# Performance work log

Measured on AMD Instinct MI355X. Metric: run time of the kernel, lower is better.

Reference implementation:

```python
import math
import jax, jax.numpy as jnp
import numpy as np

B, T, C = 2, 2048, 1024
H, Ca = 16, 64


def setup_inputs() -> dict:
    key = jax.random.key(0)
    ks = jax.random.split(key, 5)
    # kaiming-uniform-ish scale for weights
    wb = 1.0 / math.sqrt(C)
    return {
        "x": jax.random.normal(ks[0], (B, T, C), dtype=jnp.float32),
        "w_q": jax.random.uniform(ks[1], (H, C, Ca), jnp.float32, -wb, wb),
        "w_k": jax.random.uniform(ks[2], (H, C, Ca), jnp.float32, -wb, wb),
        "w_v": jax.random.uniform(ks[3], (H, C, Ca), jnp.float32, -wb, wb),
        "w_o": jax.random.uniform(ks[4], (C, C), jnp.float32, -wb, wb),
    }


def reference(x, w_q, w_k, w_v, w_o):
    # x: [B,T,C]; w_q/w_k/w_v: [H,C,Ca]; w_o: [C,C]
    scale = 1.0 / math.sqrt(w_q.shape[-1])
    q = jnp.einsum("btc,hca->bhta", x, w_q)  # [B,H,T,Ca]
    k = jnp.einsum("btc,hca->bhta", x, w_k)
    v = jnp.einsum("btc,hca->bhta", x, w_v)
    s = jnp.einsum("bhta,bhsa->bhts", q, k)  # [B,H,T,T]
    # faithful to original: mask where tril(s)==0, scale applied after masking
    s_hat = jnp.where(jnp.tril(s) == 0, -jnp.inf, s * scale)
    a = jax.nn.softmax(s_hat, axis=-1)
    y = jnp.einsum("bhts,bhsa->bhta", a, v)  # [B,H,T,Ca]
    y_cat = y.transpose(0, 2, 1, 3).reshape(x.shape)  # [B,T,C]
    return y_cat @ w_o
```

## Files before the change

### kernel.cpp

```cpp
#include <hip/hip_runtime.h>
#include <stdint.h>

#define Bc 2
#define Tc 2048
#define Cn 1024
#define Hc 16
#define CAc 64

typedef __attribute__((ext_vector_type(8))) short short8;
typedef __attribute__((ext_vector_type(4))) float f32x4;

__device__ __forceinline__ unsigned short f2bf(float f) {
    unsigned int u = __builtin_bit_cast(unsigned int, f);
    return (unsigned short)((u + 0x7fffu + ((u >> 16) & 1u)) >> 16);
}

__device__ __forceinline__ void async_cp16(const unsigned short* g, unsigned short* l) {
    __builtin_amdgcn_global_load_lds(
        (const __attribute__((address_space(1))) unsigned int*)g,
        (__attribute__((address_space(3))) unsigned int*)l,
        16, 0, 0);
}

__global__ __launch_bounds__(256) void detect_dtype(
    const unsigned short* __restrict__ x, int* __restrict__ flag)
{
    __shared__ int cnt;
    if (threadIdx.x == 0) cnt = 0;
    __syncthreads();
    int c = 0;
#pragma unroll
    for (int i = 0; i < 8; i++) {
        int idx = (threadIdx.x * 8 + i) * 2;
        unsigned short u = x[idx];
        int e = (u >> 7) & 0xFF;
        if (e >= 0x68 && e <= 0x90) c++;
    }
    atomicAdd(&cnt, c);
    __syncthreads();
    if (threadIdx.x == 0) *flag = (cnt > 1024) ? 1 : 0;
}

__global__ __launch_bounds__(256) void convert_x(
    const void* __restrict__ xin, unsigned short* __restrict__ xb,
    const int* __restrict__ flag)
{
    int idx = (blockIdx.x * 256 + threadIdx.x) * 4;
    if (*flag) {
        *(uint2*)(&xb[idx]) = *(const uint2*)((const unsigned short*)xin + idx);
    } else {
        const float* xf = (const float*)xin;
        float4 v = *(const float4*)(xf + idx);
        union { unsigned short s[4]; uint2 u; } p;
        p.s[0] = f2bf(v.x); p.s[1] = f2bf(v.y); p.s[2] = f2bf(v.z); p.s[3] = f2bf(v.w);
        *(uint2*)(&xb[idx]) = p.u;
    }
}

__device__ __forceinline__ unsigned short ld_elem(const void* base, size_t off, int isbf) {
    return isbf ? ((const unsigned short*)base)[off] : f2bf(((const float*)base)[off]);
}

__global__ __launch_bounds__(256) void transpose_weights(
    const void* __restrict__ wq, const void* __restrict__ wk,
    const void* __restrict__ wv, const void* __restrict__ wo,
    unsigned short* __restrict__ wT, unsigned short* __restrict__ woT,
    const int* __restrict__ flag)
{
    const int isbf = *flag;
    __shared__ unsigned short tile[32][33];
    const int bx = blockIdx.x;
    const int t = threadIdx.x;
    const int tx = t & 31, ty = t >> 5;
    const void* src;
    unsigned short* dst;
    int R, Cw, r0, c0;
    if (bx < 3072) {
        int g = bx >> 6;
        int rem = bx & 63;
        int ct = rem >> 1;
        int at = rem & 1;
        int proj = g >> 4, h = g & 15;
        const void* wsel = (proj == 0) ? wq : ((proj == 1) ? wk : wv);
        src = isbf ? (const void*)((const unsigned short*)wsel + (size_t)h * Cn * CAc)
                   : (const void*)((const float*)wsel + (size_t)h * Cn * CAc);
        dst = wT + (size_t)g * CAc * Cn;
        R = Cn; Cw = CAc; r0 = ct * 32; c0 = at * 32;
    } else {
        int rem = bx - 3072;
        src = wo; dst = woT;
        R = Cn; Cw = Cn;
        r0 = (rem >> 5) * 32; c0 = (rem & 31) * 32;
    }
#pragma unroll
    for (int j = 0; j < 4; j++)
        tile[ty + j * 8][tx] = ld_elem(src, (size_t)(r0 + ty + j * 8) * Cw + c0 + tx, isbf);
    __syncthreads();
#pragma unroll
    for (int j = 0; j < 4; j++)
        dst[(size_t)(c0 + ty + j * 8) * R + r0 + tx] = tile[tx][ty + j * 8];
}

template <int MODE>
__global__ __launch_bounds__(256) void gemm128(
    const unsigned short* __restrict__ Amat,
    const unsigned short* __restrict__ Bt,
    void* __restrict__ o0,
    unsigned short* __restrict__ o1,
    unsigned short* __restrict__ o2,
    const int* __restrict__ flag)
{
    __shared__ alignas(16) unsigned short Al[2][128 * 32];
    __shared__ alignas(16) unsigned short Bl[2][128 * 32];
    const int tid = threadIdx.x;
    const int wave = tid >> 6, lane = tid & 63;
    const int l15 = lane & 15, quad = lane >> 4;
    const int mBase = blockIdx.y * 128, nBase = blockIdx.x * 128;
    const int mOff = (wave & 1) * 64, nOff = (wave >> 1) * 64;

    const int srow = lane >> 2;
    const int sgc  = (lane & 3) ^ (srow & 3);
    const int sw = (quad ^ (l15 & 3)) * 8;

    f32x4 acc[4][4];
#pragma unroll
    for (int i = 0; i < 4; i++)
#pragma unroll
        for (int j = 0; j < 4; j++)
            acc[i][j] = (f32x4){0.f, 0.f, 0.f, 0.f};

#pragma unroll
    for (int t = 0; t < 2; t++) {
        int rl = wave * 32 + t * 16;
        async_cp16(Amat + (size_t)(mBase + rl + srow) * Cn + sgc * 8, &Al[0][rl * 32]);
        async_cp16(Bt   + (size_t)(nBase + rl + srow) * Cn + sgc * 8, &Bl[0][rl * 32]);
    }
    __syncthreads();

    for (int kk = 0; kk < 32; kk++) {
        const int cur = kk & 1;
        if (kk < 31) {
            const int k1 = (kk + 1) * 32;
#pragma unroll
            for (int t = 0; t < 2; t++) {
                int rl = wave * 32 + t * 16;
                async_cp16(Amat + (size_t)(mBase + rl + srow) * Cn + k1 + sgc * 8, &Al[1 - cur][rl * 32]);
                async_cp16(Bt   + (size_t)(nBase + rl + srow) * Cn + k1 + sgc * 8, &Bl[1 - cur][rl * 32]);
            }
        }
        short8 af[4], bfr[4];
#pragma unroll
        for (int i = 0; i < 4; i++)
            af[i] = *(const short8*)(&Al[cur][(mOff + i * 16 + l15) * 32 + sw]);
#pragma unroll
        for (int j = 0; j < 4; j++)
            bfr[j] = *(const short8*)(&Bl[cur][(nOff + j * 16 + l15) * 32 + sw]);
#pragma unroll
        for (int i = 0; i < 4; i++)
#pragma unroll
            for (int j = 0; j < 4; j++)
                acc[i][j] = __builtin_amdgcn_mfma_f32_16x16x32_bf16(af[i], bfr[j], acc[i][j], 0, 0, 0);
        __syncthreads();
    }

    if constexpr (MODE == 0) {
#pragma unroll
        for (int i = 0; i < 4; i++) {
            int m0 = mBase + mOff + i * 16 + quad * 4;
            int b = m0 >> 11, t0 = m0 & (Tc - 1);
#pragma unroll
            for (int j = 0; j < 4; j++) {
                int n = nBase + nOff + j * 16 + l15;
                int proj = n >> 10, h = (n >> 6) & 15, a = n & 63;
                if (proj == 2) {
                    union { unsigned short s[4]; uint2 v; } pk;
#pragma unroll
                    for (int r = 0; r < 4; r++) pk.s[r] = f2bf(acc[i][j][r]);
                    *(uint2*)(&o2[((size_t)(b * Hc + h) * CAc + a) * Tc + t0]) = pk.v;
                } else {
                    unsigned short* dst = (proj == 0) ? (unsigned short*)o0 : o1;
                    size_t base = ((size_t)(b * Hc + h) * Tc + t0) * CAc + a;
#pragma unroll
                    for (int r = 0; r < 4; r++)
                        dst[base + (size_t)r * CAc] = f2bf(acc[i][j][r]);
                }
            }
        }
    } else {
        const int isbf = *flag;
#pragma unroll
        for (int i = 0; i < 4; i++) {
            int m0 = mBase + mOff + i * 16 + quad * 4;
#pragma unroll
            for (int j = 0; j < 4; j++) {
                int n = nBase + nOff + j * 16 + l15;
                if (isbf) {
#pragma unroll
                    for (int r = 0; r < 4; r++)
                        ((unsigned short*)o0)[(size_t)(m0 + r) * Cn + n] = f2bf(acc[i][j][r]);
                } else {
#pragma unroll
                    for (int r = 0; r < 4; r++)
                        ((float*)o0)[(size_t)(m0 + r) * Cn + n] = acc[i][j][r];
                }
            }
        }
    }
}

__global__ __launch_bounds__(256) void attn_pair(
    const unsigned short* __restrict__ q,
    const unsigned short* __restrict__ k,
    const unsigned short* __restrict__ vT,
    unsigned short* __restrict__ y)
{
    __shared__ alignas(16) unsigned short Kl[2][64 * 64];
    __shared__ alignas(16) unsigned short Vl[2][64 * 64];
    const int LDP = 72;
    __shared__ alignas(16) unsigned short Pl[4][16 * LDP];
    const int bx = blockIdx.x;
    const int pr = bx & 15, bh = bx >> 4;
    const int h = bh & 15, b = bh >> 4;
    const int qt1 = pr, qt2 = 31 - pr;
    const int tid = threadIdx.x;
    const int wave = tid >> 6, lane = tid & 63;
    const int l15 = lane & 15, quad = lane >> 4;
    const int m0w1 = qt1 * 64 + wave * 16;
    const int m0w2 = qt2 * 64 + wave * 16;
    const size_t bhoff = (size_t)(b * Hc + h);
    const unsigned short* qh = q + bhoff * Tc * CAc;
    const unsigned short* kh = k + bhoff * Tc * CAc;
    const unsigned short* vh = vT + bhoff * CAc * Tc;

    const int srow = (lane >> 3);
    const int sgc  = (lane & 7) ^ srow;
    const int h7 = l15 & 7;
    const int sw0 = ((quad ^ h7) << 3);
    const int sw1 = (((4 + quad) ^ h7) << 3);

    short8 qf1[2], qf2[2];
#pragma unroll
    for (int s = 0; s < 2; s++) {
        qf1[s] = *(const short8*)(&qh[(size_t)(m0w1 + l15) * CAc + s * 32 + quad * 8]);
        qf2[s] = *(const short8*)(&qh[(size_t)(m0w2 + l15) * CAc + s * 32 + quad * 8]);
    }

    f32x4 oacc1[4], oacc2[4], osum1, osum2;
#pragma unroll
    for (int j2 = 0; j2 < 4; j2++) {
        oacc1[j2] = (f32x4){0.f, 0.f, 0.f, 0.f};
        oacc2[j2] = (f32x4){0.f, 0.f, 0.f, 0.f};
    }
    osum1 = (f32x4){0.f, 0.f, 0.f, 0.f};
    osum2 = (f32x4){0.f, 0.f, 0.f, 0.f};

    const unsigned short ONE = 0x3F80;
    short8 ones;
#pragma unroll
    for (int i = 0; i < 8; i++) ones[i] = (short)ONE;

    unsigned short* Pw = &Pl[wave][0];

#pragma unroll
    for (int t = 0; t < 2; t++) {
        int rl = wave * 16 + t * 8;
        async_cp16(kh + (size_t)(rl + srow) * CAc + sgc * 8, &Kl[0][rl * 64]);
        async_cp16(vh + (size_t)(rl + srow) * Tc  + sgc * 8, &Vl[0][rl * 64]);
    }
    __syncthreads();

    for (int kt = 0; kt <= qt2; kt++) {
        const int k0 = kt * 64;
        const int cur = kt & 1;
        const bool act1 = (kt <= qt1);
        if (kt < qt2) {
            const unsigned short* kg = kh + (size_t)(k0 + 64) * CAc;
            const unsigned short* vg = vh + (k0 + 64);
#pragma unroll
            for (int t = 0; t < 2; t++) {
                int rl = wave * 16 + t * 8;
                async_cp16(kg + (size_t)(rl + srow) * CAc + sgc * 8, &Kl[1 - cur][rl * 64]);
                async_cp16(vg + (size_t)(rl + srow) * Tc  + sgc * 8, &Vl[1 - cur][rl * 64]);
            }
        }
        const unsigned short* Kc = Kl[cur];
        const unsigned short* Vc = Vl[cur];

        float s1[4][4], s2[4][4];
#pragma unroll
        for (int j = 0; j < 4; j++) {
            short8 kf0 = *(const short8*)(&Kc[(j * 16 + l15) * 64 + sw0]);
            short8 kf1 = *(const short8*)(&Kc[(j * 16 + l15) * 64 + sw1]);
            f32x4 z2 = (f32x4){0.f, 0.f, 0.f, 0.f};
            z2 = __builtin_amdgcn_mfma_f32_16x16x32_bf16(kf0, qf2[0], z2, 0, 0, 0);
            z2 = __builtin_amdgcn_mfma_f32_16x16x32_bf16(kf1, qf2[1], z2, 0, 0, 0);
#pragma unroll
            for (int r = 0; r < 4; r++) s2[j][r] = z2[r];
            if (act1) {
                f32x4 z1 = (f32x4){0.f, 0.f, 0.f, 0.f};
                z1 = __builtin_amdgcn_mfma_f32_16x16x32_bf16(kf0, qf1[0], z1, 0, 0, 0);
                z1 = __builtin_amdgcn_mfma_f32_16x16x32_bf16(kf1, qf1[1], z1, 0, 0, 0);
#pragma unroll
                for (int r = 0; r < 4; r++) s1[j][r] = z1[r];
            }
        }

        if (kt == qt2) {
            int tg = m0w2 + l15;
#pragma unroll
            for (int j = 0; j < 4; j++)
#pragma unroll
                for (int r = 0; r < 4; r++) {
                    int sg = k0 + j * 16 + quad * 4 + r;
                    s2[j][r] = (sg <= tg) ? __expf(s2[j][r] * 0.125f) : 0.f;
                }
        } else {
#pragma unroll
            for (int j = 0; j < 4; j++)
#pragma unroll
                for (int r = 0; r < 4; r++)
                    s2[j][r] = __expf(s2[j][r] * 0.125f);
        }
        if (act1) {
            if (kt == qt1) {
                int tg = m0w1 + l15;
#pragma unroll
                for (int j = 0; j < 4; j++)
#pragma unroll
                    for (int r = 0; r < 4; r++) {
                        int sg = k0 + j * 16 + quad * 4 + r;
                        s1[j][r] = (sg <= tg) ? __expf(s1[j][r] * 0.125f) : 0.f;
                    }
            } else {
#pragma unroll
                for (int j = 0; j < 4; j++)
#pragma unroll
                    for (int r = 0; r < 4; r++)
                        s1[j][r] = __expf(s1[j][r] * 0.125f);
            }
        }

        short8 pa2[2], pa1[2];
#pragma unroll
        for (int j = 0; j < 4; j++) {
            union { unsigned int d[2]; uint2 v; } pk;
            pk.d[0] = (unsigned int)f2bf(s2[j][0]) | ((unsigned int)f2bf(s2[j][1]) << 16);
            pk.d[1] = (unsigned int)f2bf(s2[j][2]) | ((unsigned int)f2bf(s2[j][3]) << 16);
            *(uint2*)(&Pw[l15 * LDP + j * 16 + quad * 4]) = pk.v;
        }
#pragma unroll
        for (int c = 0; c < 2; c++)
            pa2[c] = *(const short8*)(&Pw[l15 * LDP + c * 32 + quad * 8]);
        if (act1) {
#pragma unroll
            for (int j = 0; j < 4; j++) {
                union { unsigned int d[2]; uint2 v; } pk;
                pk.d[0] = (unsigned int)f2bf(s1[j][0]) | ((unsigned int)f2bf(s1[j][1]) << 16);
                pk.d[1] = (unsigned int)f2bf(s1[j][2]) | ((unsigned int)f2bf(s1[j][3]) << 16);
                *(uint2*)(&Pw[l15 * LDP + j * 16 + quad * 4]) = pk.v;
            }
#pragma unroll
            for (int c = 0; c < 2; c++)
                pa1[c] = *(const short8*)(&Pw[l15 * LDP + c * 32 + quad * 8]);
        }

#pragma unroll
        for (int c = 0; c < 2; c++) {
#pragma unroll
            for (int j2 = 0; j2 < 4; j2++) {
                short8 vb = *(const short8*)(&Vc[(j2 * 16 + l15) * 64 + (c ? sw1 : sw0)]);
                oacc2[j2] = __builtin_amdgcn_mfma_f32_16x16x32_bf16(pa2[c], vb, oacc2[j2], 0, 0, 0);
                if (act1)
                    oacc1[j2] = __builtin_amdgcn_mfma_f32_16x16x32_bf16(pa1[c], vb, oacc1[j2], 0, 0, 0);
            }
            osum2 = __builtin_amdgcn_mfma_f32_16x16x32_bf16(pa2[c], ones, osum2, 0, 0, 0);
            if (act1)
                osum1 = __builtin_amdgcn_mfma_f32_16x16x32_bf16(pa1[c], ones, osum1, 0, 0, 0);
        }
        __syncthreads();
    }

    float ri1[4], ri2[4];
#pragma unroll
    for (int r = 0; r < 4; r++) { ri1[r] = 1.0f / osum1[r]; ri2[r] = 1.0f / osum2[r]; }
#pragma unroll
    for (int j2 = 0; j2 < 4; j2++) {
#pragma unroll
        for (int r = 0; r < 4; r++) {
            int t1 = m0w1 + quad * 4 + r;
            int t2 = m0w2 + quad * 4 + r;
            y[((size_t)b * Tc + t1) * Cn + h * CAc + j2 * 16 + l15] = f2bf(oacc1[j2][r] * ri1[r]);
            y[((size_t)b * Tc + t2) * Cn + h * CAc + j2 * 16 + l15] = f2bf(oacc2[j2][r] * ri2[r]);
        }
    }
}

extern "C" void kernel_launch(void* const* d_in, const int* in_sizes, int n_in,
                              void* d_out, int out_size, void* d_ws, size_t ws_size,
                              hipStream_t stream) {
    const void* x  = d_in[0];
    const void* wq = d_in[1];
    const void* wk = d_in[2];
    const void* wv = d_in[3];
    const void* wo = d_in[4];
    char* ws = (char*)d_ws;
    int* flag = (int*)(ws);
    unsigned short* wT  = (unsigned short*)(ws + ((size_t)1 << 20));
    unsigned short* woT = (unsigned short*)(ws + ((size_t)7 << 20));
    unsigned short* xb  = (unsigned short*)(ws + ((size_t)9 << 20));
    unsigned short* qb  = (unsigned short*)(ws + ((size_t)17 << 20));
    unsigned short* kb  = (unsigned short*)(ws + ((size_t)25 << 20));
    unsigned short* vTb = (unsigned short*)(ws + ((size_t)33 << 20));
    unsigned short* yb  = (unsigned short*)(ws + ((size_t)41 << 20));

    detect_dtype<<<dim3(1), dim3(256), 0, stream>>>((const unsigned short*)x, flag);
    convert_x<<<dim3(4096), dim3(256), 0, stream>>>(x, xb, flag);
    transpose_weights<<<dim3(4096), dim3(256), 0, stream>>>(wq, wk, wv, wo, wT, woT, flag);
    gemm128<0><<<dim3(24, 32), dim3(256), 0, stream>>>(xb, wT, qb, kb, vTb, flag);
    attn_pair<<<dim3(512), dim3(256), 0, stream>>>(qb, kb, vTb, yb);
    gemm128<1><<<dim3(8, 32), dim3(256), 0, stream>>>(yb, woT, d_out, nullptr, nullptr, flag);
}
```

Before: 211.8 us.

## Merge prep kernels, shrink output GEMM tile, truncate softmax probabilities to bf16

Fuses the x conversion and weight transpose into one launch to save a kernel launch and its gap. The output projection now uses 64x128 tiles, giving 512 blocks instead of 256 so more of the GPU's compute units are filled. In attention, probabilities are packed to bf16 by truncation instead of round-to-nearest, which cuts ALU work in the inner loop but adds a small downward bias to the probabilities.

```diff
diff --git a/kernel.cpp b/kernel.cpp
--- a/kernel.cpp
+++ b/kernel.cpp
@@ -14,6 +14,11 @@
     unsigned int u = __builtin_bit_cast(unsigned int, f);
     return (unsigned short)((u + 0x7fffu + ((u >> 16) & 1u)) >> 16);
 }
+__device__ __forceinline__ unsigned int pack_trunc(float a, float b) {
+    unsigned int ua = __builtin_bit_cast(unsigned int, a);
+    unsigned int ub = __builtin_bit_cast(unsigned int, b);
+    return (ua >> 16) | (ub & 0xFFFF0000u);
+}
 
 __device__ __forceinline__ void async_cp16(const unsigned short* g, unsigned short* l) {
     __builtin_amdgcn_global_load_lds(
@@ -41,43 +46,42 @@
     if (threadIdx.x == 0) *flag = (cnt > 1024) ? 1 : 0;
 }
 
-__global__ __launch_bounds__(256) void convert_x(
-    const void* __restrict__ xin, unsigned short* __restrict__ xb,
-    const int* __restrict__ flag)
-{
-    int idx = (blockIdx.x * 256 + threadIdx.x) * 4;
-    if (*flag) {
-        *(uint2*)(&xb[idx]) = *(const uint2*)((const unsigned short*)xin + idx);
-    } else {
-        const float* xf = (const float*)xin;
-        float4 v = *(const float4*)(xf + idx);
-        union { unsigned short s[4]; uint2 u; } p;
-        p.s[0] = f2bf(v.x); p.s[1] = f2bf(v.y); p.s[2] = f2bf(v.z); p.s[3] = f2bf(v.w);
-        *(uint2*)(&xb[idx]) = p.u;
-    }
-}
-
 __device__ __forceinline__ unsigned short ld_elem(const void* base, size_t off, int isbf) {
     return isbf ? ((const unsigned short*)base)[off] : f2bf(((const float*)base)[off]);
 }
 
-__global__ __launch_bounds__(256) void transpose_weights(
+__global__ __launch_bounds__(256) void prep(
+    const void* __restrict__ xin, unsigned short* __restrict__ xb,
     const void* __restrict__ wq, const void* __restrict__ wk,
     const void* __restrict__ wv, const void* __restrict__ wo,
     unsigned short* __restrict__ wT, unsigned short* __restrict__ woT,
     const int* __restrict__ flag)
 {
     const int isbf = *flag;
+    const int bx = blockIdx.x;
+    if (bx < 4096) {
+        int idx = (bx * 256 + threadIdx.x) * 4;
+        if (isbf) {
+            *(uint2*)(&xb[idx]) = *(const uint2*)((const unsigned short*)xin + idx);
+        } else {
+            const float* xf = (const float*)xin;
+            float4 v = *(const float4*)(xf + idx);
+            union { unsigned short s[4]; uint2 u; } p;
+            p.s[0] = f2bf(v.x); p.s[1] = f2bf(v.y); p.s[2] = f2bf(v.z); p.s[3] = f2bf(v.w);
+            *(uint2*)(&xb[idx]) = p.u;
+        }
+        return;
+    }
     __shared__ unsigned short tile[32][33];
-    const int bx = blockIdx.x;
     const int t = threadIdx.x;
     const int tx = t & 31, ty = t >> 5;
     const void* src;
     unsigned short* dst;
     int R, Cw, r0, c0;
-    if (bx < 3072) {
-        int g = bx >> 6;
-        int rem = bx & 63;
+    if (bx < 7168) {
+        int rem0 = bx - 4096;
+        int g = rem0 >> 6;
+        int rem = rem0 & 63;
         int ct = rem >> 1;
         int at = rem & 1;
         int proj = g >> 4, h = g & 15;
@@ -87,7 +91,7 @@
         dst = wT + (size_t)g * CAc * Cn;
         R = Cn; Cw = CAc; r0 = ct * 32; c0 = at * 32;
     } else {
-        int rem = bx - 3072;
+        int rem = bx - 7168;
         src = wo; dst = woT;
         R = Cn; Cw = Cn;
         r0 = (rem >> 5) * 32; c0 = (rem & 31) * 32;
@@ -101,14 +105,12 @@
         dst[(size_t)(c0 + ty + j * 8) * R + r0 + tx] = tile[tx][ty + j * 8];
 }
 
-template <int MODE>
-__global__ __launch_bounds__(256) void gemm128(
+__global__ __launch_bounds__(256) void gemm_qkv(
     const unsigned short* __restrict__ Amat,
     const unsigned short* __restrict__ Bt,
-    void* __restrict__ o0,
+    unsigned short* __restrict__ o0,
     unsigned short* __restrict__ o1,
-    unsigned short* __restrict__ o2,
-    const int* __restrict__ flag)
+    unsigned short* __restrict__ o2)
 {
     __shared__ alignas(16) unsigned short Al[2][128 * 32];
     __shared__ alignas(16) unsigned short Bl[2][128 * 32];
@@ -163,46 +165,108 @@
         __syncthreads();
     }
 
-    if constexpr (MODE == 0) {
-#pragma unroll
-        for (int i = 0; i < 4; i++) {
-            int m0 = mBase + mOff + i * 16 + quad * 4;
-            int b = m0 >> 11, t0 = m0 & (Tc - 1);
-#pragma unroll
-            for (int j = 0; j < 4; j++) {
-                int n = nBase + nOff + j * 16 + l15;
-                int proj = n >> 10, h = (n >> 6) & 15, a = n & 63;
-                if (proj == 2) {
-                    union { unsigned short s[4]; uint2 v; } pk;
-#pragma unroll
-                    for (int r = 0; r < 4; r++) pk.s[r] = f2bf(acc[i][j][r]);
-                    *(uint2*)(&o2[((size_t)(b * Hc + h) * CAc + a) * Tc + t0]) = pk.v;
-                } else {
-                    unsigned short* dst = (proj == 0) ? (unsigned short*)o0 : o1;
-                    size_t base = ((size_t)(b * Hc + h) * Tc + t0) * CAc + a;
-#pragma unroll
-                    for (int r = 0; r < 4; r++)
-                        dst[base + (size_t)r * CAc] = f2bf(acc[i][j][r]);
-                }
-            }
-        }
-    } else {
-        const int isbf = *flag;
-#pragma unroll
-        for (int i = 0; i < 4; i++) {
-            int m0 = mBase + mOff + i * 16 + quad * 4;
-#pragma unroll
-            for (int j = 0; j < 4; j++) {
-                int n = nBase + nOff + j * 16 + l15;
-                if (isbf) {
-#pragma unroll
-                    for (int r = 0; r < 4; r++)
-                        ((unsigned short*)o0)[(size_t)(m0 + r) * Cn + n] = f2bf(acc[i][j][r]);
-                } else {
-#pragma unroll
-                    for (int r = 0; r < 4; r++)
-                        ((float*)o0)[(size_t)(m0 + r) * Cn + n] = acc[i][j][r];
-                }
+#pragma unroll
+    for (int i = 0; i < 4; i++) {
+        int m0 = mBase + mOff + i * 16 + quad * 4;
+        int b = m0 >> 11, t0 = m0 & (Tc - 1);
+#pragma unroll
+        for (int j = 0; j < 4; j++) {
+            int n = nBase + nOff + j * 16 + l15;
+            int proj = n >> 10, h = (n >> 6) & 15, a = n & 63;
+            if (proj == 2) {
+                union { unsigned short s[4]; uint2 v; } pk;
+#pragma unroll
+                for (int r = 0; r < 4; r++) pk.s[r] = f2bf(acc[i][j][r]);
+                *(uint2*)(&o2[((size_t)(b * Hc + h) * CAc + a) * Tc + t0]) = pk.v;
+            } else {
+                unsigned short* dst = (proj == 0) ? o0 : o1;
+                size_t base = ((size_t)(b * Hc + h) * Tc + t0) * CAc + a;
+#pragma unroll
+                for (int r = 0; r < 4; r++)
+                    dst[base + (size_t)r * CAc] = f2bf(acc[i][j][r]);
+            }
+        }
+    }
+}
+
+__global__ __launch_bounds__(256) void gemm_out(
+    const unsigned short* __restrict__ Amat,
+    const unsigned short* __restrict__ Bt,
+    void* __restrict__ o0,
+    const int* __restrict__ flag)
+{
+    __shared__ alignas(16) unsigned short Al[2][64 * 32];
+    __shared__ alignas(16) unsigned short Bl[2][128 * 32];
+    const int tid = threadIdx.x;
+    const int wave = tid >> 6, lane = tid & 63;
+    const int l15 = lane & 15, quad = lane >> 4;
+    const int mBase = blockIdx.y * 64, nBase = blockIdx.x * 128;
+    const int mOff = (wave & 1) * 32, nOff = (wave >> 1) * 64;
+
+    const int srow = lane >> 2;
+    const int sgc  = (lane & 3) ^ (srow & 3);
+    const int sw = (quad ^ (l15 & 3)) * 8;
+
+    f32x4 acc[2][4];
+#pragma unroll
+    for (int i = 0; i < 2; i++)
+#pragma unroll
+        for (int j = 0; j < 4; j++)
+            acc[i][j] = (f32x4){0.f, 0.f, 0.f, 0.f};
+
+    {
+        int rlA = wave * 16;
+        async_cp16(Amat + (size_t)(mBase + rlA + srow) * Cn + sgc * 8, &Al[0][rlA * 32]);
+#pragma unroll
+        for (int t = 0; t < 2; t++) {
+            int rlB = wave * 32 + t * 16;
+            async_cp16(Bt + (size_t)(nBase + rlB + srow) * Cn + sgc * 8, &Bl[0][rlB * 32]);
+        }
+    }
+    __syncthreads();
+
+    for (int kk = 0; kk < 32; kk++) {
+        const int cur = kk & 1;
+        if (kk < 31) {
+            const int k1 = (kk + 1) * 32;
+            int rlA = wave * 16;
+            async_cp16(Amat + (size_t)(mBase + rlA + srow) * Cn + k1 + sgc * 8, &Al[1 - cur][rlA * 32]);
+#pragma unroll
+            for (int t = 0; t < 2; t++) {
+                int rlB = wave * 32 + t * 16;
+                async_cp16(Bt + (size_t)(nBase + rlB + srow) * Cn + k1 + sgc * 8, &Bl[1 - cur][rlB * 32]);
+            }
+        }
+        short8 af[2], bfr[4];
+#pragma unroll
+        for (int i = 0; i < 2; i++)
+            af[i] = *(const short8*)(&Al[cur][(mOff + i * 16 + l15) * 32 + sw]);
+#pragma unroll
+        for (int j = 0; j < 4; j++)
+            bfr[j] = *(const short8*)(&Bl[cur][(nOff + j * 16 + l15) * 32 + sw]);
+#pragma unroll
+        for (int i = 0; i < 2; i++)
+#pragma unroll
+            for (int j = 0; j < 4; j++)
+                acc[i][j] = __builtin_amdgcn_mfma_f32_16x16x32_bf16(af[i], bfr[j], acc[i][j], 0, 0, 0);
+        __syncthreads();
+    }
+
+    const int isbf = *flag;
+#pragma unroll
+    for (int i = 0; i < 2; i++) {
+        int m0 = mBase + mOff + i * 16 + quad * 4;
+#pragma unroll
+        for (int j = 0; j < 4; j++) {
+            int n = nBase + nOff + j * 16 + l15;
+            if (isbf) {
+#pragma unroll
+                for (int r = 0; r < 4; r++)
+                    ((unsigned short*)o0)[(size_t)(m0 + r) * Cn + n] = f2bf(acc[i][j][r]);
+            } else {
+#pragma unroll
+                for (int r = 0; r < 4; r++)
+                    ((float*)o0)[(size_t)(m0 + r) * Cn + n] = acc[i][j][r];
             }
         }
     }
@@ -343,10 +407,10 @@
         short8 pa2[2], pa1[2];
 #pragma unroll
         for (int j = 0; j < 4; j++) {
-            union { unsigned int d[2]; uint2 v; } pk;
-            pk.d[0] = (unsigned int)f2bf(s2[j][0]) | ((unsigned int)f2bf(s2[j][1]) << 16);
-            pk.d[1] = (unsigned int)f2bf(s2[j][2]) | ((unsigned int)f2bf(s2[j][3]) << 16);
-            *(uint2*)(&Pw[l15 * LDP + j * 16 + quad * 4]) = pk.v;
+            uint2 v;
+            v.x = pack_trunc(s2[j][0], s2[j][1]);
+            v.y = pack_trunc(s2[j][2], s2[j][3]);
+            *(uint2*)(&Pw[l15 * LDP + j * 16 + quad * 4]) = v;
         }
 #pragma unroll
         for (int c = 0; c < 2; c++)
@@ -354,10 +418,10 @@
         if (act1) {
 #pragma unroll
             for (int j = 0; j < 4; j++) {
-                union { unsigned int d[2]; uint2 v; } pk;
-                pk.d[0] = (unsigned int)f2bf(s1[j][0]) | ((unsigned int)f2bf(s1[j][1]) << 16);
-                pk.d[1] = (unsigned int)f2bf(s1[j][2]) | ((unsigned int)f2bf(s1[j][3]) << 16);
-                *(uint2*)(&Pw[l15 * LDP + j * 16 + quad * 4]) = pk.v;
+                uint2 v;
+                v.x = pack_trunc(s1[j][0], s1[j][1]);
+                v.y = pack_trunc(s1[j][2], s1[j][3]);
+                *(uint2*)(&Pw[l15 * LDP + j * 16 + quad * 4]) = v;
             }
 #pragma unroll
             for (int c = 0; c < 2; c++)
@@ -414,9 +478,8 @@
     unsigned short* yb  = (unsigned short*)(ws + ((size_t)41 << 20));
 
     detect_dtype<<<dim3(1), dim3(256), 0, stream>>>((const unsigned short*)x, flag);
-    convert_x<<<dim3(4096), dim3(256), 0, stream>>>(x, xb, flag);
-    transpose_weights<<<dim3(4096), dim3(256), 0, stream>>>(wq, wk, wv, wo, wT, woT, flag);
-    gemm128<0><<<dim3(24, 32), dim3(256), 0, stream>>>(xb, wT, qb, kb, vTb, flag);
+    prep<<<dim3(8192), dim3(256), 0, stream>>>(x, xb, wq, wk, wv, wo, wT, woT, flag);
+    gemm_qkv<<<dim3(24, 32), dim3(256), 0, stream>>>(xb, wT, qb, kb, vTb);
     attn_pair<<<dim3(512), dim3(256), 0, stream>>>(qb, kb, vTb, yb);
-    gemm128<1><<<dim3(8, 32), dim3(256), 0, stream>>>(yb, woT, d_out, nullptr, nullptr, flag);
-}
+    gemm_out<<<dim3(8, 64), dim3(256), 0, stream>>>(yb, woT, d_out, flag);
+}
```

Result: faster. 204.0 us (-3.6%).
